# Kernel tuning notes

Hardware: AMD Instinct MI355X
Metric: run time of the kernel (lower is better)

The kernel has to match this reference:

```python
import jax, jax.numpy as jnp
import numpy as np

NUM_ENTITIES = 100000
NUM_RELATIONS = 16
EMBED_DIM = 128
NUM_LAYERS = 2
NUM_HEADS = 4
B = 4096
K = 64


def setup_inputs() -> dict:
    key = jax.random.key(0)
    ks = jax.random.split(key, 10)
    D = EMBED_DIM
    s = 1.0 / np.sqrt(D)
    return {
        "drug_entity_indices": jax.random.randint(ks[0], (B,), 0, NUM_ENTITIES),
        "adj_entity": jax.random.randint(ks[1], (B, K), 0, NUM_ENTITIES),
        "adj_relation": jax.random.randint(ks[2], (B, K), 0, NUM_RELATIONS),
        "edge_weights": jax.random.uniform(ks[3], (B, K), dtype=jnp.float32),
        "E": jax.random.normal(ks[4], (NUM_ENTITIES, D), dtype=jnp.float32) * 0.02,
        "W_rel": jax.random.normal(ks[5], (NUM_LAYERS, NUM_RELATIONS, D, D), dtype=jnp.float32) * s,
        "res_W": jax.random.normal(ks[6], (NUM_LAYERS, D, D), dtype=jnp.float32) * s,
        "res_b": jnp.zeros((NUM_LAYERS, D), dtype=jnp.float32),
        "in_proj_w": jax.random.normal(ks[7], (3 * D, D), dtype=jnp.float32) * s,
        "in_proj_b": jnp.zeros((3 * D,), dtype=jnp.float32),
        "out_proj_w": jax.random.normal(ks[8], (D, D), dtype=jnp.float32) * s,
        "out_proj_b": jnp.zeros((D,), dtype=jnp.float32),
    }


def reference(drug_entity_indices, adj_entity, adj_relation, edge_weights,
              E, W_rel, res_W, res_b, in_proj_w, in_proj_b, out_proj_w, out_proj_b):
    D = E.shape[1]
    H = NUM_HEADS
    dh = D // H

    x = E[drug_entity_indices][None, :, :]  # [1,B,D]

    # Per-edge relation one-hot * edge weight; exact same math as the torch
    # per-relation masked loop (sum and matmul commute over the K axis).
    wr = jax.nn.one_hot(adj_relation, NUM_RELATIONS, dtype=edge_weights.dtype) * edge_weights[:, :, None]  # [B,K,R]
    neigh = E[adj_entity]                               # [B,K,D] gather
    agg = jnp.einsum('bkd,bkr->brd', neigh, wr)         # [B,R,D]

    outs = []
    for l in range(NUM_LAYERS):
        msgs = jnp.einsum('brd,rde->be', agg, W_rel[l])[None]          # [1,B,D]
        resid = jnp.einsum('lbd,ed->lbe', x, res_W[l]) + res_b[l]      # Linear(x)
        x = jax.nn.relu(x + msgs + resid)
        outs.append(x)

    attn_in = jnp.concatenate(outs, axis=0)             # [L,B,D]
    Lq, Bn, _ = attn_in.shape
    qkv = attn_in @ in_proj_w.T + in_proj_b             # [L,B,3D]
    q, k, v = jnp.split(qkv, 3, axis=-1)

    def heads(t):
        return t.reshape(Lq, Bn, H, dh).transpose(1, 2, 0, 3)  # [B,H,L,dh]

    q, k, v = heads(q), heads(k), heads(v)
    scores = jnp.einsum('bhqd,bhkd->bhqk', q, k) / jnp.sqrt(jnp.asarray(dh, q.dtype))
    a = jax.nn.softmax(scores, axis=-1)
    o = jnp.einsum('bhqk,bhkd->bhqd', a, v).transpose(2, 0, 1, 3).reshape(Lq, Bn, D)
    attn_out = o @ out_proj_w.T + out_proj_b            # [L,B,D]
    return attn_out.mean(axis=0)                        # [B,D]
```

## Files before the change

kernel.cpp:

```cpp
#include <hip/hip_runtime.h>

#define B_N 4096
#define KE 64
#define R_N 16

typedef unsigned short u16;
typedef __attribute__((ext_vector_type(4))) float f4;
typedef __attribute__((ext_vector_type(4))) float f32x4;
typedef __attribute__((ext_vector_type(8))) short bf16x8;

__device__ __forceinline__ float b2f(u16 u) {
  union { unsigned int i; float f; } z; z.i = ((unsigned int)u) << 16; return z.f;
}
__device__ __forceinline__ u16 f2b(float f) {
  union { float f; unsigned int i; } z; z.f = f;
  unsigned int r = (z.i + 0x7FFFu + ((z.i >> 16) & 1u)) >> 16;
  return (u16)r;
}

template<int LOG2SLOTS, int NISS>
__device__ __forceinline__ void stage_tile(const u16* gbase, size_t gstride,
                                           u16* lds, int t) {
#pragma unroll
  for (int s = 0; s < NISS; ++s) {
    const int lin = s * 256 + t;
    const int r = lin >> LOG2SLOTS;
    const int p = lin & ((1 << LOG2SLOTS) - 1);
    const int lsl = p ^ (r & 7);
    const u16* src = gbase + (size_t)r * gstride + (lsl << 3);
    __builtin_amdgcn_global_load_lds(
        (const __attribute__((address_space(1))) void*)src,
        (__attribute__((address_space(3))) void*)(lds + (size_t)lin * 8), 16, 0, 0);
  }
}

__global__ __launch_bounds__(256) void k_prep_wcat(const float* __restrict__ W_rel,
                                                   u16* __restrict__ WcatT) {
  __shared__ __align__(16) u16 T[128][130];
  const int lr = blockIdx.x;
  const int t = threadIdx.x;
  const float* src = W_rel + (size_t)lr * 128 * 128;
#pragma unroll
  for (int s = 0; s < 16; ++s) {
    const int idx4 = s * 256 + t;
    const int d = idx4 >> 5, e4 = idx4 & 31;
    const f4 v = *(const f4*)(src + (size_t)d * 128 + e4 * 4);
#pragma unroll
    for (int j = 0; j < 4; ++j) T[d][e4 * 4 + j] = f2b(v[j]);
  }
  __syncthreads();
  const int l = lr >> 4, r = lr & 15;
  const int e = t >> 1, d0 = (t & 1) * 64;
  u16* dst = WcatT + (size_t)(l * 128 + e) * 2048 + r * 128 + d0;
#pragma unroll
  for (int j8 = 0; j8 < 8; ++j8) {
    bf16x8 w;
#pragma unroll
    for (int i = 0; i < 8; ++i) w[i] = (short)T[d0 + j8 * 8 + i][e];
    *(bf16x8*)(dst + j8 * 8) = w;
  }
}

__global__ __launch_bounds__(256) void k_prep_cast(const float* __restrict__ res_W,
                                                   const float* __restrict__ in_w,
                                                   const float* __restrict__ out_w,
                                                   u16* __restrict__ resWT,
                                                   u16* __restrict__ in_wT,
                                                   u16* __restrict__ out_wT) {
  const int i = blockIdx.x * 256 + threadIdx.x;
  if (i < 32768) resWT[i] = f2b(res_W[i]);
  else if (i < 81920) in_wT[i - 32768] = f2b(in_w[i - 32768]);
  else out_wT[i - 81920] = f2b(out_w[i - 81920]);
}

__global__ __launch_bounds__(128) void k_gather(
    const int* __restrict__ didx, const int* __restrict__ adj_e,
    const int* __restrict__ adj_r, const float* __restrict__ ew,
    const float* __restrict__ E, u16* __restrict__ agg, u16* __restrict__ x0) {
  __shared__ __align__(16) float sa[4][R_N][128];
  const int b = blockIdx.x;
  const int t = threadIdx.x;
  const int g = t >> 5, ln = t & 31;
  float* flat = &sa[0][0][0];
#pragma unroll
  for (int i = 0; i < 64; ++i) flat[t + 128 * i] = 0.f;
  __syncthreads();
  const int base = b * KE;
#pragma unroll 2
  for (int kg = 0; kg < 16; ++kg) {
    const int k = (kg << 2) | g;
    const int e = adj_e[base + k];
    const int r = adj_r[base + k];
    const float wk = ew[base + k];
    const f4 v = *(const f4*)(E + (size_t)e * 128 + (ln << 2));
    float* dst = &sa[g][r][ln << 2];
    dst[0] += wk * v[0]; dst[1] += wk * v[1];
    dst[2] += wk * v[2]; dst[3] += wk * v[3];
  }
  __syncthreads();
  const int o0 = t * 16;
  const int r = o0 >> 7, d0 = o0 & 127;
#pragma unroll
  for (int j2 = 0; j2 < 2; ++j2) {
    bf16x8 w;
#pragma unroll
    for (int i = 0; i < 8; ++i) {
      const int d = d0 + j2 * 8 + i;
      w[i] = (short)f2b(sa[0][r][d] + sa[1][r][d] + sa[2][r][d] + sa[3][r][d]);
    }
    *(bf16x8*)(agg + (size_t)b * 2048 + o0 + j2 * 8) = w;
  }
  x0[(size_t)b * 128 + t] = f2b(E[(size_t)didx[b] * 128 + t]);
}

__global__ __launch_bounds__(256) void k_msgs(const u16* __restrict__ agg,
                                              const u16* __restrict__ WcatT,
                                              float* __restrict__ Cp) {
  __shared__ __align__(16) u16 As[2][128 * 64];
  __shared__ __align__(16) u16 Bs[2][128 * 64];
  const int t = threadIdx.x;
  const int bm = blockIdx.x, bn = blockIdx.y, sp = blockIdx.z;
  const int w = t >> 6, l = t & 63;
  const int wm = w >> 1, wn = w & 1;
  const int l16 = l & 15, l4 = l >> 4;
  const u16* Abase = agg + (size_t)bm * 128 * 2048 + sp * 512;
  const u16* Bbase = WcatT + (size_t)bn * 128 * 2048 + sp * 512;
  f32x4 acc[4][4] = {};

  stage_tile<3, 4>(Abase, 2048, As[0], t);
  stage_tile<3, 4>(Bbase, 2048, Bs[0], t);
  __syncthreads();
#pragma unroll 1
  for (int c = 0; c < 8; ++c) {
    const int cur = c & 1;
    if (c < 7) {
      stage_tile<3, 4>(Abase + (c + 1) * 64, 2048, As[cur ^ 1], t);
      stage_tile<3, 4>(Bbase + (c + 1) * 64, 2048, Bs[cur ^ 1], t);
    }
#pragma unroll
    for (int ks = 0; ks < 2; ++ks) {
      bf16x8 a[4], b[4];
#pragma unroll
      for (int mi = 0; mi < 4; ++mi) {
        const int r = wm * 64 + mi * 16 + l16;
        const int phys = ((ks << 2) + l4) ^ (r & 7);
        a[mi] = *(const bf16x8*)&As[cur][r * 64 + phys * 8];
      }
#pragma unroll
      for (int ni = 0; ni < 4; ++ni) {
        const int r = wn * 64 + ni * 16 + l16;
        const int phys = ((ks << 2) + l4) ^ (r & 7);
        b[ni] = *(const bf16x8*)&Bs[cur][r * 64 + phys * 8];
      }
#pragma unroll
      for (int mi = 0; mi < 4; ++mi)
#pragma unroll
        for (int ni = 0; ni < 4; ++ni)
          acc[mi][ni] =
              __builtin_amdgcn_mfma_f32_16x16x32_bf16(a[mi], b[ni], acc[mi][ni], 0, 0, 0);
    }
    __syncthreads();
  }
  float* cp = Cp + (size_t)sp * B_N * 256;
#pragma unroll
  for (int mi = 0; mi < 4; ++mi) {
    const int m0 = bm * 128 + wm * 64 + mi * 16 + l4 * 4;
#pragma unroll
    for (int ni = 0; ni < 4; ++ni) {
      const int n = bn * 128 + wn * 64 + ni * 16 + l16;
#pragma unroll
      for (int j = 0; j < 4; ++j) cp[(size_t)(m0 + j) * 256 + n] = acc[mi][ni][j];
    }
  }
}

template<int MODE>
__global__ __launch_bounds__(256) void k_small(const u16* __restrict__ A,
                                               const u16* __restrict__ BT,
                                               const float* __restrict__ bias,
                                               void* __restrict__ Cout, int ldc,
                                               const float* __restrict__ msgsP,
                                               int mcol0) {
  __shared__ __align__(16) u16 As[64 * 128];
  __shared__ __align__(16) u16 Bs[64 * 128];
  const int t = threadIdx.x;
  const int row0 = blockIdx.x * 64;
  const int n0 = blockIdx.y * 64;
  const int w = t >> 6, l = t & 63;
  const int wm = w >> 1, wn = w & 1;
  const int l16 = l & 15, l4 = l >> 4;
  stage_tile<4, 4>(A + (size_t)row0 * 128, 128, As, t);
  stage_tile<4, 4>(BT + (size_t)n0 * 128, 128, Bs, t);
  __syncthreads();
  f32x4 acc[2][2] = {};
#pragma unroll
  for (int ks = 0; ks < 4; ++ks) {
    bf16x8 a[2], b[2];
#pragma unroll
    for (int mi = 0; mi < 2; ++mi) {
      const int r = wm * 32 + mi * 16 + l16;
      const int phys = ((ks << 2) + l4) ^ (r & 7);
      a[mi] = *(const bf16x8*)&As[r * 128 + phys * 8];
    }
#pragma unroll
    for (int ni = 0; ni < 2; ++ni) {
      const int r = wn * 32 + ni * 16 + l16;
      const int phys = ((ks << 2) + l4) ^ (r & 7);
      b[ni] = *(const bf16x8*)&Bs[r * 128 + phys * 8];
    }
#pragma unroll
    for (int mi = 0; mi < 2; ++mi)
#pragma unroll
      for (int ni = 0; ni < 2; ++ni)
        acc[mi][ni] =
            __builtin_amdgcn_mfma_f32_16x16x32_bf16(a[mi], b[ni], acc[mi][ni], 0, 0, 0);
  }
  const size_t BSZ = (size_t)B_N * 256;
#pragma unroll
  for (int mi = 0; mi < 2; ++mi) {
#pragma unroll
    for (int ni = 0; ni < 2; ++ni) {
      const int n = n0 + wn * 32 + ni * 16 + l16;
#pragma unroll
      for (int j = 0; j < 4; ++j) {
        const int m = row0 + wm * 32 + mi * 16 + l4 * 4 + j;
        float v = acc[mi][ni][j] + bias[n];
        if (MODE == 2) {
          const size_t mo = (size_t)m * 256 + mcol0 + n;
          v += b2f(A[(size_t)m * 128 + n]) + msgsP[mo] + msgsP[BSZ + mo] +
               msgsP[2 * BSZ + mo] + msgsP[3 * BSZ + mo];
          v = fmaxf(v, 0.f);
        }
        if (MODE == 1)
          ((float*)Cout)[(size_t)m * ldc + n] = v;
        else
          ((u16*)Cout)[(size_t)m * ldc + n] = f2b(v);
      }
    }
  }
}

__global__ __launch_bounds__(256) void k_attn(const u16* __restrict__ qkv,
                                              u16* __restrict__ om) {
  const int t = blockIdx.x * 256 + threadIdx.x;
  const int b = t >> 7, d = t & 127;
  const u16* p0 = qkv + (size_t)b * 384;
  const u16* p1 = qkv + (size_t)(B_N + b) * 384;
  const float q0 = b2f(p0[d]), q1 = b2f(p1[d]);
  const float k0 = b2f(p0[128 + d]), k1 = b2f(p1[128 + d]);
  const float v0 = b2f(p0[256 + d]), v1 = b2f(p1[256 + d]);
  float p00 = q0 * k0, p01 = q0 * k1, p10 = q1 * k0, p11 = q1 * k1;
#pragma unroll
  for (int m = 16; m >= 1; m >>= 1) {
    p00 += __shfl_xor(p00, m);
    p01 += __shfl_xor(p01, m);
    p10 += __shfl_xor(p10, m);
    p11 += __shfl_xor(p11, m);
  }
  const float sc = 0.17677669529663687f;
  const float s00 = p00 * sc, s01 = p01 * sc, s10 = p10 * sc, s11 = p11 * sc;
  const float m0 = fmaxf(s00, s01);
  const float e00 = __expf(s00 - m0), e01 = __expf(s01 - m0);
  const float o0 = (e00 * v0 + e01 * v1) / (e00 + e01);
  const float m1 = fmaxf(s10, s11);
  const float e10 = __expf(s10 - m1), e11 = __expf(s11 - m1);
  const float o1 = (e10 * v0 + e11 * v1) / (e10 + e11);
  om[t] = f2b(0.5f * (o0 + o1));
}

extern "C" void kernel_launch(void* const* d_in, const int* in_sizes, int n_in,
                              void* d_out, int out_size, void* d_ws, size_t ws_size,
                              hipStream_t stream) {
  const int* didx = (const int*)d_in[0];
  const int* adj_e = (const int*)d_in[1];
  const int* adj_r = (const int*)d_in[2];
  const float* ew = (const float*)d_in[3];
  const float* E = (const float*)d_in[4];
  const float* W_rel = (const float*)d_in[5];
  const float* res_W = (const float*)d_in[6];
  const float* res_b = (const float*)d_in[7];
  const float* in_w = (const float*)d_in[8];
  const float* in_b = (const float*)d_in[9];
  const float* out_w = (const float*)d_in[10];
  const float* out_b = (const float*)d_in[11];

  char* ws = (char*)d_ws;
  u16* agg = (u16*)(ws + 0);
  u16* WcatT = (u16*)(ws + 16777216);
  u16* resWT = (u16*)(ws + 17825792);
  u16* in_wT = (u16*)(ws + 17891328);
  u16* out_wT = (u16*)(ws + 17989632);
  u16* x0 = (u16*)(ws + 18022400);
  u16* xs = (u16*)(ws + 19070976);
  u16* qkv = (u16*)(ws + 21168128);
  u16* om = (u16*)(ws + 27459584);
  float* Cp = (float*)(ws + 28508160);

  k_prep_wcat<<<32, 256, 0, stream>>>(W_rel, WcatT);
  k_prep_cast<<<384, 256, 0, stream>>>(res_W, in_w, out_w, resWT, in_wT, out_wT);
  k_gather<<<B_N, 128, 0, stream>>>(didx, adj_e, adj_r, ew, E, agg, x0);
  k_msgs<<<dim3(32, 2, 4), 256, 0, stream>>>(agg, WcatT, Cp);

  k_small<2><<<dim3(64, 2), 256, 0, stream>>>(x0, resWT, res_b, xs, 128, Cp, 0);
  k_small<2><<<dim3(64, 2), 256, 0, stream>>>(xs, resWT + 16384, res_b + 128,
                                              xs + (size_t)B_N * 128, 128, Cp, 128);
  k_small<0><<<dim3(128, 6), 256, 0, stream>>>(xs, in_wT, in_b, qkv, 384, nullptr, 0);
  k_attn<<<(B_N * 128) / 256, 256, 0, stream>>>(qkv, om);
  k_small<1><<<dim3(64, 2), 256, 0, stream>>>(om, out_wT, out_b, d_out, 128, nullptr, 0);
}
```

Measured before the change: 177.1 us.

## Parallelize gather across all 64 edges with LDS atomics; split weight transpose prep

The gather kernel now uses 256 threads so each edge's embedding row is loaded by four threads at once. Per-edge contributions are accumulated into a single shared per-relation buffer with LDS atomicAdd, replacing four private partial buffers, a 16-iteration loop and a final reduction. Read and write offsets are rotated per edge to spread LDS bank conflicts. Separately, the W_rel transpose/cast prep runs on 8x more blocks, each handling a 16-column chunk with a much smaller LDS tile. The gather change exposes more memory-level parallelism but pays for LDS float atomics and contention when several edges share a relation.

Measured after the change: 309.6 us. 1.75x slower.

```diff
diff --git a/kernel.cpp b/kernel.cpp
--- a/kernel.cpp
+++ b/kernel.cpp
@@ -36,29 +36,25 @@
 
 __global__ __launch_bounds__(256) void k_prep_wcat(const float* __restrict__ W_rel,
                                                    u16* __restrict__ WcatT) {
-  __shared__ __align__(16) u16 T[128][130];
+  __shared__ __align__(16) u16 T[16][136];
   const int lr = blockIdx.x;
+  const int c = blockIdx.y;
   const int t = threadIdx.x;
   const float* src = W_rel + (size_t)lr * 128 * 128;
-#pragma unroll
-  for (int s = 0; s < 16; ++s) {
-    const int idx4 = s * 256 + t;
-    const int d = idx4 >> 5, e4 = idx4 & 31;
-    const f4 v = *(const f4*)(src + (size_t)d * 128 + e4 * 4);
-#pragma unroll
-    for (int j = 0; j < 4; ++j) T[d][e4 * 4 + j] = f2b(v[j]);
+  const int d = t >> 1, h = t & 1;
+#pragma unroll
+  for (int hh = 0; hh < 2; ++hh) {
+    const f4 v = *(const f4*)(src + (size_t)d * 128 + c * 16 + h * 8 + hh * 4);
+#pragma unroll
+    for (int j = 0; j < 4; ++j) T[h * 8 + hh * 4 + j][d] = f2b(v[j]);
   }
   __syncthreads();
   const int l = lr >> 4, r = lr & 15;
-  const int e = t >> 1, d0 = (t & 1) * 64;
-  u16* dst = WcatT + (size_t)(l * 128 + e) * 2048 + r * 128 + d0;
-#pragma unroll
-  for (int j8 = 0; j8 < 8; ++j8) {
-    bf16x8 w;
-#pragma unroll
-    for (int i = 0; i < 8; ++i) w[i] = (short)T[d0 + j8 * 8 + i][e];
-    *(bf16x8*)(dst + j8 * 8) = w;
-  }
+  const int e_l = t >> 4, d0 = (t & 15) * 8;
+  bf16x8 w;
+#pragma unroll
+  for (int i = 0; i < 8; ++i) w[i] = (short)T[e_l][d0 + i];
+  *(bf16x8*)(WcatT + (size_t)(l * 128 + c * 16 + e_l) * 2048 + r * 128 + d0) = w;
 }
 
 __global__ __launch_bounds__(256) void k_prep_cast(const float* __restrict__ res_W,
@@ -73,44 +69,47 @@
   else out_wT[i - 81920] = f2b(out_w[i - 81920]);
 }
 
-__global__ __launch_bounds__(128) void k_gather(
+__global__ __launch_bounds__(256) void k_gather(
     const int* __restrict__ didx, const int* __restrict__ adj_e,
     const int* __restrict__ adj_r, const float* __restrict__ ew,
     const float* __restrict__ E, u16* __restrict__ agg, u16* __restrict__ x0) {
-  __shared__ __align__(16) float sa[4][R_N][128];
+  __shared__ __align__(16) float sa[R_N][128];
   const int b = blockIdx.x;
   const int t = threadIdx.x;
-  const int g = t >> 5, ln = t & 31;
-  float* flat = &sa[0][0][0];
-#pragma unroll
-  for (int i = 0; i < 64; ++i) flat[t + 128 * i] = 0.f;
-  __syncthreads();
-  const int base = b * KE;
-#pragma unroll 2
-  for (int kg = 0; kg < 16; ++kg) {
-    const int k = (kg << 2) | g;
-    const int e = adj_e[base + k];
-    const int r = adj_r[base + k];
-    const float wk = ew[base + k];
-    const f4 v = *(const f4*)(E + (size_t)e * 128 + (ln << 2));
-    float* dst = &sa[g][r][ln << 2];
-    dst[0] += wk * v[0]; dst[1] += wk * v[1];
-    dst[2] += wk * v[2]; dst[3] += wk * v[3];
-  }
-  __syncthreads();
-  const int o0 = t * 16;
-  const int r = o0 >> 7, d0 = o0 & 127;
-#pragma unroll
-  for (int j2 = 0; j2 < 2; ++j2) {
+  float* flat = &sa[0][0];
+#pragma unroll
+  for (int i = 0; i < 8; ++i) flat[t + 256 * i] = 0.f;
+  __syncthreads();
+  const int k = t >> 2, q = t & 3;
+  const int e = adj_e[b * KE + k];
+  const int r = adj_r[b * KE + k];
+  const float wk = ew[b * KE + k];
+  const float* strip = E + (size_t)e * 128 + q * 32;
+  f4 v[8];
+#pragma unroll
+  for (int i = 0; i < 8; ++i) v[i] = *(const f4*)(strip + (((i + k) & 7) << 2));
+  float* dst = &sa[r][q * 32];
+#pragma unroll
+  for (int i = 0; i < 8; ++i) {
+    const int p0 = ((i + k) & 7) << 2;
+#pragma unroll
+    for (int j = 0; j < 4; ++j) atomicAdd(&dst[p0 + j], wk * v[i][j]);
+  }
+  __syncthreads();
+  {
+    const int o0 = t * 8;
     bf16x8 w;
 #pragma unroll
-    for (int i = 0; i < 8; ++i) {
-      const int d = d0 + j2 * 8 + i;
-      w[i] = (short)f2b(sa[0][r][d] + sa[1][r][d] + sa[2][r][d] + sa[3][r][d]);
-    }
-    *(bf16x8*)(agg + (size_t)b * 2048 + o0 + j2 * 8) = w;
-  }
-  x0[(size_t)b * 128 + t] = f2b(E[(size_t)didx[b] * 128 + t]);
+    for (int i = 0; i < 8; ++i) w[i] = (short)f2b(flat[o0 + i]);
+    *(bf16x8*)(agg + (size_t)b * 2048 + o0) = w;
+  }
+  if (t < 16) {
+    const float* src = E + (size_t)didx[b] * 128 + t * 8;
+    bf16x8 w;
+#pragma unroll
+    for (int i = 0; i < 8; ++i) w[i] = (short)f2b(src[i]);
+    *(bf16x8*)(x0 + (size_t)b * 128 + t * 8) = w;
+  }
 }
 
 __global__ __launch_bounds__(256) void k_msgs(const u16* __restrict__ agg,
@@ -296,9 +295,9 @@
   u16* om = (u16*)(ws + 27459584);
   float* Cp = (float*)(ws + 28508160);
 
-  k_prep_wcat<<<32, 256, 0, stream>>>(W_rel, WcatT);
+  k_prep_wcat<<<dim3(32, 8), 256, 0, stream>>>(W_rel, WcatT);
   k_prep_cast<<<384, 256, 0, stream>>>(res_W, in_w, out_w, resWT, in_wT, out_wT);
-  k_gather<<<B_N, 128, 0, stream>>>(didx, adj_e, adj_r, ew, E, agg, x0);
+  k_gather<<<B_N, 256, 0, stream>>>(didx, adj_e, adj_r, ew, E, agg, x0);
   k_msgs<<<dim3(32, 2, 4), 256, 0, stream>>>(agg, WcatT, Cp);
 
   k_small<2><<<dim3(64, 2), 256, 0, stream>>>(x0, resWT, res_b, xs, 128, Cp, 0);
```
